# Kernel tuning notes

Hardware: AMD Instinct MI355X
Metric: run time of the kernel (lower is better)

## Reference

```python
import jax, jax.numpy as jnp
import numpy as np

L, B, S, D, H, DH, I, M = 4, 8, 1024, 256, 8, 32, 1024, 4
EPS = 1e-12


def setup_inputs() -> dict:
    key = jax.random.key(0)
    ks = jax.random.split(key, 12)

    def nrm(k, shape, scale=0.02):
        return jax.random.normal(k, shape, jnp.float32) * scale

    x = jax.random.randint(ks[0], (B, S), 0, M + 1)  # POVM outcome tokens + start token

    # sinusoidal positional encoding buffer [S, D]
    pos = np.arange(S, dtype=np.float32)[:, None]
    div = np.exp(np.arange(0, D, 2, dtype=np.float32) * (-np.log(10000.0) / D))
    pe_np = np.zeros((S, D), np.float32)
    pe_np[:, 0::2] = np.sin(pos * div)
    pe_np[:, 1::2] = np.cos(pos * div)

    return {
        "x": x,
        "emb_w": nrm(ks[1], (M + 1, D)),
        "pe": jnp.asarray(pe_np),
        "q_w": nrm(ks[2], (L, D, D)), "q_b": jnp.zeros((L, D)),
        "k_w": nrm(ks[3], (L, D, D)), "k_b": jnp.zeros((L, D)),
        "v_w": nrm(ks[4], (L, D, D)), "v_b": jnp.zeros((L, D)),
        "o_w": nrm(ks[5], (L, D, D)), "o_b": jnp.zeros((L, D)),
        "ln1_g": jnp.ones((L, D)), "ln1_b": jnp.zeros((L, D)),
        "f1_w": nrm(ks[6], (L, I, D)), "f1_b": jnp.zeros((L, I)),
        "f2_w": nrm(ks[7], (L, D, I)), "f2_b": jnp.zeros((L, D)),
        "ln2_g": jnp.ones((L, D)), "ln2_b": jnp.zeros((L, D)),
        "out_w": nrm(ks[8], (M, D)), "out_b": jnp.zeros((M,)),
    }


def _ln(x, g, b):
    m = jnp.mean(x, -1, keepdims=True)
    v = jnp.mean((x - m) ** 2, -1, keepdims=True)
    return g * (x - m) * jax.lax.rsqrt(v + EPS) + b


def reference(x, emb_w, pe, q_w, q_b, k_w, k_b, v_w, v_b, o_w, o_b,
              ln1_g, ln1_b, f1_w, f1_b, f2_w, f2_b, ln2_g, ln2_b,
              out_w, out_b):
    h = emb_w[x] + pe[None, :S, :]                       # [B,S,D]
    mask = jnp.triu(jnp.full((S, S), -1e9, jnp.float32), 1)  # causal look-ahead
    scale = 1.0 / jnp.sqrt(jnp.float32(DH))

    for l in range(L):
        # multi-head self-attention (torch Linear: x @ W.T + b)
        q = (h @ q_w[l].T + q_b[l]).reshape(B, S, H, DH)
        k = (h @ k_w[l].T + k_b[l]).reshape(B, S, H, DH)
        v = (h @ v_w[l].T + v_b[l]).reshape(B, S, H, DH)
        scores = jnp.einsum('bqhd,bkhd->bhqk', q, k) * scale + mask
        probs = jax.nn.softmax(scores, axis=-1)
        ctx = jnp.einsum('bhqk,bkhd->bqhd', probs, v).reshape(B, S, D)
        attn_out = _ln(ctx @ o_w[l].T + o_b[l] + h, ln1_g[l], ln1_b[l])
        # feed-forward sublayer
        ff = jax.nn.gelu(attn_out @ f1_w[l].T + f1_b[l], approximate=False)
        h = _ln(ff @ f2_w[l].T + f2_b[l] + attn_out, ln2_g[l], ln2_b[l])

    logits = h @ out_w.T + out_b                          # [B,S,M]
    return logits
```

## Files before the change

kernel.cpp:

```cpp
#include <hip/hip_runtime.h>
#include <cstdint>
#include <cstddef>

#define SS 1024
#define DD 256

typedef unsigned short u16;
typedef __bf16 bf16x8 __attribute__((ext_vector_type(8)));
typedef float f32x4 __attribute__((ext_vector_type(4)));
typedef unsigned short us4 __attribute__((ext_vector_type(4)));

typedef __attribute__((address_space(3))) void lds_void_t;
typedef __attribute__((address_space(1))) const void gvoid_t;

__device__ __forceinline__ u16 f2bf(float f) {
  unsigned u = __builtin_bit_cast(unsigned, f);
  u += 0x7fffu + ((u >> 16) & 1u);
  return (u16)(u >> 16);
}
__device__ __forceinline__ u16 f2bf_fast(float f) {
  unsigned u = __builtin_bit_cast(unsigned, f) + 0x8000u;
  return (u16)(u >> 16);
}
__device__ __forceinline__ float bf2f(u16 h) {
  return __builtin_bit_cast(float, ((unsigned)h) << 16);
}
__device__ __forceinline__ void gld_lds16(const void* g, void* l) {
  __builtin_amdgcn_global_load_lds((gvoid_t*)g, (lds_void_t*)l, 16, 0, 0);
}
template <int CTRL>
__device__ __forceinline__ float dppf(float x) {
  int i = __builtin_bit_cast(int, x);
  int r = __builtin_amdgcn_update_dpp(i, i, CTRL, 0xf, 0xf, false);
  return __builtin_bit_cast(float, r);
}
__device__ __forceinline__ float row_sum16(float v) {
  v += dppf<0x121>(v);
  v += dppf<0x122>(v);
  v += dppf<0x124>(v);
  v += dppf<0x128>(v);
  return v;
}

struct CvtArgs {
  const float* src[9];
  void* dst[9];
  int n4[9];
  int bf[9];
};

__global__ __launch_bounds__(256) void cvt_kernel(CvtArgs a) {
  int g = blockIdx.y;
  int i = blockIdx.x * 256 + threadIdx.x;
  if (i >= a.n4[g]) return;
  float4 v = ((const float4*)a.src[g])[i];
  if (a.bf[g]) {
    us4 o; o.x = f2bf(v.x); o.y = f2bf(v.y); o.z = f2bf(v.z); o.w = f2bf(v.w);
    ((us4*)a.dst[g])[i] = o;
  } else {
    ((float4*)a.dst[g])[i] = v;
  }
}

__global__ __launch_bounds__(256)
void embed_kernel(const int* __restrict__ x, const float* __restrict__ emb,
                  const float* __restrict__ pe, u16* __restrict__ h) {
  int wave = threadIdx.x >> 6, lane = threadIdx.x & 63;
  int row = blockIdx.x * 4 + wave;
  int s = row & (SS - 1);
  int tok = x[row];
  float4 e = *(const float4*)(emb + (size_t)tok * DD + lane * 4);
  float4 p = *(const float4*)(pe + (size_t)s * DD + lane * 4);
  us4 o; o.x = f2bf(e.x + p.x); o.y = f2bf(e.y + p.y);
  o.z = f2bf(e.z + p.z); o.w = f2bf(e.w + p.w);
  *(us4*)(h + (size_t)row * DD + lane * 4) = o;
}

enum { EPI_BIAS = 0, EPI_GELU = 1 };

#define Q_SCALE (0.17677669529663689f * 1.4426950408889634f)

template <int BM, int BN, int EPI, bool QKV>
__global__ __launch_bounds__(256)
void gemm_kernel(const u16* __restrict__ A, const u16* __restrict__ W,
                 const float* __restrict__ bias, void* __restrict__ outp,
                 u16* __restrict__ vt_out, int M, int N, int K) {
  const int n0 = blockIdx.x * BN;
  const int m0 = blockIdx.y * BM;
  const int tid = threadIdx.x;
  const int lane = tid & 63;
  const int l15 = lane & 15;
  const int quad = lane >> 4;
  const int wave = tid >> 6;
  const int wrow = wave >> 1, wcol = wave & 1;
  constexpr int WN = BN / 2;
  constexpr int NT = WN / 16;

  const u16* Wp = W;
  const float* biasp = bias;
  u16* out16 = (u16*)outp;
  int zid = 0;
  if constexpr (QKV) {
    zid = blockIdx.z;
    Wp += (size_t)zid * 262144;
    biasp += (size_t)zid * 1024;
    out16 += (size_t)zid * 2097152;
  }

  __shared__ __align__(16) u16 lds[(BM + BN) * 64];
  char* ldsA = (char*)lds;
  char* ldsB = (char*)lds + BM * 128;

  const f32x4 fzero = {0.f, 0.f, 0.f, 0.f};
  f32x4 acc[4][NT];
#pragma unroll
  for (int i = 0; i < 4; ++i)
#pragma unroll
    for (int j = 0; j < NT; ++j) acc[i][j] = fzero;

  for (int kb = 0; kb < K; kb += 64) {
    __syncthreads();
#pragma unroll
    for (int r = 0; r < BM * 8 / 256; ++r) {
      int c = r * 256 + tid;
      int row = c >> 3, slot = c & 7;
      int gc = slot ^ (row & 7);
      gld_lds16((const char*)(A + (size_t)(m0 + row) * K + kb) + gc * 16,
                ldsA + c * 16);
    }
#pragma unroll
    for (int r = 0; r < BN * 8 / 256; ++r) {
      int c = r * 256 + tid;
      int row = c >> 3, slot = c & 7;
      int gc = slot ^ (row & 7);
      gld_lds16((const char*)(Wp + (size_t)(n0 + row) * K + kb) + gc * 16,
                ldsB + c * 16);
    }
    __syncthreads();
#pragma unroll
    for (int kk = 0; kk < 2; ++kk) {
      bf16x8 af[4], bfr[NT];
#pragma unroll
      for (int i = 0; i < 4; ++i) {
        int row = wrow * 64 + i * 16 + l15;
        int slot = (kk * 4 + quad) ^ (row & 7);
        af[i] = *(const bf16x8*)(ldsA + row * 128 + slot * 16);
      }
#pragma unroll
      for (int j = 0; j < NT; ++j) {
        int row = wcol * WN + j * 16 + l15;
        int slot = (kk * 4 + quad) ^ (row & 7);
        bfr[j] = *(const bf16x8*)(ldsB + row * 128 + slot * 16);
      }
#pragma unroll
      for (int i = 0; i < 4; ++i)
#pragma unroll
        for (int j = 0; j < NT; ++j)
          acc[i][j] = __builtin_amdgcn_mfma_f32_16x16x32_bf16(af[i], bfr[j],
                                                              acc[i][j], 0, 0, 0);
    }
  }
  if (QKV && zid == 2) {
#pragma unroll
    for (int i = 0; i < 4; ++i) {
      int rbase = m0 + wrow * 64 + i * 16 + quad * 4;
      int bidx = rbase >> 10, s0 = rbase & 1023;
#pragma unroll
      for (int j = 0; j < NT; ++j) {
        int col = n0 + wcol * WN + j * 16 + l15;
        float bj = biasp[col];
        us4 o;
        o.x = f2bf(acc[i][j][0] + bj);
        o.y = f2bf(acc[i][j][1] + bj);
        o.z = f2bf(acc[i][j][2] + bj);
        o.w = f2bf(acc[i][j][3] + bj);
        *(us4*)(vt_out + ((size_t)(bidx * 8 + (col >> 5)) * 32 + (col & 31)) * SS + s0) = o;
      }
    }
    return;
  }
  const float oscale = (QKV && zid == 0) ? Q_SCALE : 1.0f;
#pragma unroll
  for (int i = 0; i < 4; ++i) {
    int rbase = m0 + wrow * 64 + i * 16 + quad * 4;
#pragma unroll
    for (int j = 0; j < NT; ++j) {
      int col = n0 + wcol * WN + j * 16 + l15;
      float bj = biasp[col];
#pragma unroll
      for (int r = 0; r < 4; ++r) {
        size_t idx = (size_t)(rbase + r) * N + col;
        float v = acc[i][j][r] + bj;
        if constexpr (EPI == EPI_GELU) {
          v = 0.5f * v * (1.0f + erff(v * 0.70710678118654752f));
          out16[idx] = f2bf(v);
        } else {
          out16[idx] = f2bf(v * oscale);
        }
      }
    }
  }
}

template <int K, bool LAST>
__global__ __launch_bounds__(256)
void gemmln_kernel(const u16* __restrict__ A, const u16* __restrict__ W,
                   const float* __restrict__ bias, const u16* __restrict__ res,
                   const float* __restrict__ g, const float* __restrict__ bta,
                   u16* __restrict__ out, const float* __restrict__ ow,
                   const float* __restrict__ obias, float* __restrict__ outp) {
  const int m0 = blockIdx.x * 32;
  const int tid = threadIdx.x;
  const int l15 = tid & 15;
  const int quad = (tid & 63) >> 4;
  const int wave = tid >> 6;

  __shared__ __align__(16) u16 lds[(32 + 256) * 64];
  char* ldsA = (char*)lds;
  char* ldsB = (char*)lds + 32 * 128;

  const f32x4 fzero = {0.f, 0.f, 0.f, 0.f};
  f32x4 acc[2][4];
#pragma unroll
  for (int i = 0; i < 2; ++i)
#pragma unroll
    for (int j = 0; j < 4; ++j) acc[i][j] = fzero;

  for (int kb = 0; kb < K; kb += 64) {
    __syncthreads();
    {
      int c = tid;
      int row = c >> 3, slot = c & 7;
      int gc = slot ^ (row & 7);
      gld_lds16((const char*)(A + (size_t)(m0 + row) * K + kb) + gc * 16,
                ldsA + c * 16);
    }
#pragma unroll
    for (int r = 0; r < 8; ++r) {
      int c = r * 256 + tid;
      int row = c >> 3, slot = c & 7;
      int gc = slot ^ (row & 7);
      gld_lds16((const char*)(W + (size_t)row * K + kb) + gc * 16,
                ldsB + c * 16);
    }
    __syncthreads();
#pragma unroll
    for (int kk = 0; kk < 2; ++kk) {
      bf16x8 af[2], bfr[4];
#pragma unroll
      for (int i = 0; i < 2; ++i) {
        int row = i * 16 + l15;
        int slot = (kk * 4 + quad) ^ (row & 7);
        af[i] = *(const bf16x8*)(ldsA + row * 128 + slot * 16);
      }
#pragma unroll
      for (int j = 0; j < 4; ++j) {
        int row = wave * 64 + j * 16 + l15;
        int slot = (kk * 4 + quad) ^ (row & 7);
        bfr[j] = *(const bf16x8*)(ldsB + row * 128 + slot * 16);
      }
#pragma unroll
      for (int i = 0; i < 2; ++i)
#pragma unroll
        for (int j = 0; j < 4; ++j)
          acc[i][j] = __builtin_amdgcn_mfma_f32_16x16x32_bf16(af[i], bfr[j],
                                                              acc[i][j], 0, 0, 0);
    }
  }
  float sm[2][4], sq[2][4];
#pragma unroll
  for (int i = 0; i < 2; ++i)
#pragma unroll
    for (int r = 0; r < 4; ++r) { sm[i][r] = 0.f; sq[i][r] = 0.f; }
#pragma unroll
  for (int j = 0; j < 4; ++j) {
    int col = wave * 64 + j * 16 + l15;
    float bj = bias[col];
#pragma unroll
    for (int i = 0; i < 2; ++i) {
#pragma unroll
      for (int r = 0; r < 4; ++r) {
        int grow = m0 + i * 16 + quad * 4 + r;
        float v = acc[i][j][r] + bj + bf2f(res[(size_t)grow * DD + col]);
        acc[i][j][r] = v;
        sm[i][r] += v;
        sq[i][r] += v * v;
      }
    }
  }
#pragma unroll
  for (int i = 0; i < 2; ++i)
#pragma unroll
    for (int r = 0; r < 4; ++r) {
      sm[i][r] = row_sum16(sm[i][r]);
      sq[i][r] = row_sum16(sq[i][r]);
    }
  __syncthreads();
  float* sred = (float*)lds;
  if (l15 == 0) {
#pragma unroll
    for (int i = 0; i < 2; ++i)
#pragma unroll
      for (int r = 0; r < 4; ++r) {
        int ri = i * 16 + quad * 4 + r;
        sred[wave * 64 + ri] = sm[i][r];
        sred[wave * 64 + 32 + ri] = sq[i][r];
      }
  }
  __syncthreads();
  float mean[2][4], rstd[2][4];
#pragma unroll
  for (int i = 0; i < 2; ++i)
#pragma unroll
    for (int r = 0; r < 4; ++r) {
      int ri = i * 16 + quad * 4 + r;
      float S = sred[ri] + sred[64 + ri] + sred[128 + ri] + sred[192 + ri];
      float S2 = sred[32 + ri] + sred[96 + ri] + sred[160 + ri] + sred[224 + ri];
      float mu = S * (1.f / 256.f);
      mean[i][r] = mu;
      rstd[i][r] = rsqrtf(S2 * (1.f / 256.f) - mu * mu + 1e-12f);
    }
  if constexpr (!LAST) {
#pragma unroll
    for (int j = 0; j < 4; ++j) {
      int col = wave * 64 + j * 16 + l15;
      float gj = g[col], bj = bta[col];
#pragma unroll
      for (int i = 0; i < 2; ++i)
#pragma unroll
        for (int r = 0; r < 4; ++r) {
          int grow = m0 + i * 16 + quad * 4 + r;
          float v = (acc[i][j][r] - mean[i][r]) * rstd[i][r] * gj + bj;
          out[(size_t)grow * DD + col] = f2bf(v);
        }
    }
  } else {
    float lg[2][4][4];
#pragma unroll
    for (int i = 0; i < 2; ++i)
#pragma unroll
      for (int r = 0; r < 4; ++r)
#pragma unroll
        for (int m = 0; m < 4; ++m) lg[i][r][m] = 0.f;
#pragma unroll
    for (int j = 0; j < 4; ++j) {
      int col = wave * 64 + j * 16 + l15;
      float gj = g[col], bj = bta[col];
      float wm[4];
#pragma unroll
      for (int m = 0; m < 4; ++m) wm[m] = ow[m * 256 + col];
#pragma unroll
      for (int i = 0; i < 2; ++i)
#pragma unroll
        for (int r = 0; r < 4; ++r) {
          float v = (acc[i][j][r] - mean[i][r]) * rstd[i][r] * gj + bj;
#pragma unroll
          for (int m = 0; m < 4; ++m) lg[i][r][m] += v * wm[m];
        }
    }
#pragma unroll
    for (int i = 0; i < 2; ++i)
#pragma unroll
      for (int r = 0; r < 4; ++r)
#pragma unroll
        for (int m = 0; m < 4; ++m) lg[i][r][m] = row_sum16(lg[i][r][m]);
    __syncthreads();
    float* sredh = (float*)lds;
    if (l15 == 0) {
#pragma unroll
      for (int i = 0; i < 2; ++i)
#pragma unroll
        for (int r = 0; r < 4; ++r)
#pragma unroll
          for (int m = 0; m < 4; ++m)
            sredh[wave * 128 + (i * 16 + quad * 4 + r) * 4 + m] = lg[i][r][m];
    }
    __syncthreads();
    if (tid < 128) {
      int rr = tid >> 2, m = tid & 3;
      float s = sredh[rr * 4 + m] + sredh[128 + rr * 4 + m] +
                sredh[256 + rr * 4 + m] + sredh[384 + rr * 4 + m] + obias[m];
      outp[(size_t)(m0 + rr) * 4 + m] = s;
    }
  }
}

__global__ __launch_bounds__(256)
void attn_kernel(const u16* __restrict__ Q, const u16* __restrict__ Km,
                 const u16* __restrict__ Vt, u16* __restrict__ ctx) {
  const int tid = threadIdx.x;
  const int l15 = tid & 15;
  const int quad = (tid & 63) >> 4;
  const int wave = tid >> 6;
  const int y = blockIdx.y;
  const int qt = 15 - (((int)blockIdx.x + ((y >> 4) << 2)) & 15);
  const int q0 = qt * 64;
  const int b = y >> 3, h = y & 7;
  const int q0w = q0 + wave * 16;

  __shared__ __align__(16) u16 sK[2][64 * 40];
  __shared__ __align__(16) u16 sV[2][32 * 72];
  __shared__ __align__(16) u16 sP[4][16 * 72];
  u16* sPw = sP[wave];

  bf16x8 qf = *(const bf16x8*)(Q + ((size_t)(b * SS + q0w + l15)) * DD + h * 32 + quad * 8);

  const int krow = tid >> 2, kch = tid & 3;
  const int vd = tid >> 3, vch = tid & 7;
  const u16* Kbase = Km + (size_t)(b * SS) * DD + h * 32;
  const u16* Vbase = Vt + ((size_t)y * 32 + vd) * SS;

  uint4 kreg = *(const uint4*)(Kbase + (size_t)krow * DD + kch * 8);
  uint4 vreg = *(const uint4*)(Vbase + vch * 8);

  f32x4 o0 = {0.f, 0.f, 0.f, 0.f}, o1 = {0.f, 0.f, 0.f, 0.f};
  const f32x4 fzero = {0.f, 0.f, 0.f, 0.f};
  float rs[4] = {0.f, 0.f, 0.f, 0.f};

  const int nt = q0 >> 6;
  for (int it = 0; it <= nt; ++it) {
    const int bsel = it & 1;
    *(uint4*)((char*)sK[bsel] + krow * 80 + kch * 16) = kreg;
    *(uint4*)((char*)sV[bsel] + vd * 144 + vch * 16) = vreg;
    if (it < nt) {
      int kb = (it + 1) * 64;
      kreg = *(const uint4*)(Kbase + (size_t)(kb + krow) * DD + kch * 8);
      vreg = *(const uint4*)(Vbase + kb + vch * 8);
    }
    __syncthreads();

    f32x4 s4[4];
#pragma unroll
    for (int t = 0; t < 4; ++t) {
      bf16x8 kf = *(const bf16x8*)((const char*)sK[bsel] + (t * 16 + l15) * 80 + quad * 16);
      s4[t] = __builtin_amdgcn_mfma_f32_16x16x32_bf16(qf, kf, fzero, 0, 0, 0);
    }
    if (it == nt) {
#pragma unroll
      for (int t = 0; t < 4; ++t) {
        int key = it * 64 + t * 16 + l15;
#pragma unroll
        for (int r = 0; r < 4; ++r) {
          int qr = q0w + quad * 4 + r;
          float p = exp2f(s4[t][r]);
          p = (key > qr) ? 0.f : p;
          s4[t][r] = p;
          rs[r] += p;
        }
      }
    } else {
#pragma unroll
      for (int t = 0; t < 4; ++t)
#pragma unroll
        for (int r = 0; r < 4; ++r) {
          float p = exp2f(s4[t][r]);
          s4[t][r] = p;
          rs[r] += p;
        }
    }
#pragma unroll
    for (int t = 0; t < 4; ++t)
#pragma unroll
      for (int r = 0; r < 4; ++r)
        sPw[(quad * 4 + r) * 72 + t * 16 + l15] = f2bf_fast(s4[t][r]);
#pragma unroll
    for (int kt = 0; kt < 2; ++kt) {
      bf16x8 pf = *(const bf16x8*)((char*)sPw + l15 * 144 + kt * 64 + quad * 16);
      bf16x8 v0 = *(const bf16x8*)((const char*)sV[bsel] + l15 * 144 + kt * 64 + quad * 16);
      bf16x8 v1 = *(const bf16x8*)((const char*)sV[bsel] + (16 + l15) * 144 + kt * 64 + quad * 16);
      o0 = __builtin_amdgcn_mfma_f32_16x16x32_bf16(pf, v0, o0, 0, 0, 0);
      o1 = __builtin_amdgcn_mfma_f32_16x16x32_bf16(pf, v1, o1, 0, 0, 0);
    }
  }
#pragma unroll
  for (int r = 0; r < 4; ++r) {
    float inv = 1.0f / row_sum16(rs[r]);
    int q = q0w + quad * 4 + r;
    size_t base = ((size_t)(b * SS + q)) * DD + h * 32;
    ctx[base + l15] = f2bf(o0[r] * inv);
    ctx[base + 16 + l15] = f2bf(o1[r] * inv);
  }
}

extern "C" void kernel_launch(void* const* d_in, const int* in_sizes, int n_in,
                              void* d_out, int out_size, void* d_ws, size_t ws_size,
                              hipStream_t stream) {
  const int* x = (const int*)d_in[0];
  const float* emb_w = (const float*)d_in[1];
  const float* pe = (const float*)d_in[2];
  const float* q_w = (const float*)d_in[3];
  const float* q_b = (const float*)d_in[4];
  const float* k_w = (const float*)d_in[5];
  const float* k_b = (const float*)d_in[6];
  const float* v_w = (const float*)d_in[7];
  const float* v_b = (const float*)d_in[8];
  const float* o_w = (const float*)d_in[9];
  const float* o_b = (const float*)d_in[10];
  const float* ln1_g = (const float*)d_in[11];
  const float* ln1_b = (const float*)d_in[12];
  const float* f1_w = (const float*)d_in[13];
  const float* f1_b = (const float*)d_in[14];
  const float* f2_w = (const float*)d_in[15];
  const float* f2_b = (const float*)d_in[16];
  const float* ln2_g = (const float*)d_in[17];
  const float* ln2_b = (const float*)d_in[18];
  const float* out_w = (const float*)d_in[19];
  const float* out_b = (const float*)d_in[20];
  float* out = (float*)d_out;

  char* w = (char*)d_ws;
  const size_t MB = 1ull << 20;
  u16* hb    = (u16*)(w + 0 * MB);
  u16* qb    = (u16*)(w + 4 * MB);
  u16* kbuf  = (u16*)(w + 8 * MB);
  u16* vtb   = (u16*)(w + 12 * MB);
  u16* ctxb  = (u16*)(w + 16 * MB);
  u16* attnb = (u16*)(w + 20 * MB);
  u16* ffb   = (u16*)(w + 24 * MB);
  u16* wqkv  = (u16*)(w + 48 * MB);
  u16* wo    = (u16*)(w + 50 * MB);
  u16* wf1   = (u16*)(w + 51 * MB);
  u16* wf2   = (u16*)(w + 53 * MB);
  float* bqkv = (float*)(w + 55 * MB);

  CvtArgs ca;
  ca.src[0] = q_w;  ca.dst[0] = wqkv;            ca.n4[0] = 65536;  ca.bf[0] = 1;
  ca.src[1] = k_w;  ca.dst[1] = wqkv + 262144;   ca.n4[1] = 65536;  ca.bf[1] = 1;
  ca.src[2] = v_w;  ca.dst[2] = wqkv + 524288;   ca.n4[2] = 65536;  ca.bf[2] = 1;
  ca.src[3] = o_w;  ca.dst[3] = wo;              ca.n4[3] = 65536;  ca.bf[3] = 1;
  ca.src[4] = f1_w; ca.dst[4] = wf1;             ca.n4[4] = 262144; ca.bf[4] = 1;
  ca.src[5] = f2_w; ca.dst[5] = wf2;             ca.n4[5] = 262144; ca.bf[5] = 1;
  ca.src[6] = q_b;  ca.dst[6] = bqkv;            ca.n4[6] = 256;    ca.bf[6] = 0;
  ca.src[7] = k_b;  ca.dst[7] = bqkv + 1024;     ca.n4[7] = 256;    ca.bf[7] = 0;
  ca.src[8] = v_b;  ca.dst[8] = bqkv + 2048;     ca.n4[8] = 256;    ca.bf[8] = 0;
  cvt_kernel<<<dim3(1024, 9), 256, 0, stream>>>(ca);

  embed_kernel<<<2048, 256, 0, stream>>>(x, emb_w, pe, hb);

  for (int l = 0; l < 4; ++l) {
    const size_t wofs = (size_t)l * 65536;
    const size_t fofs = (size_t)l * 262144;
    gemm_kernel<128, 64, EPI_BIAS, true><<<dim3(4, 64, 3), 256, 0, stream>>>(
        hb, wqkv + wofs, bqkv + l * 256, qb, vtb, 8192, 256, 256);
    attn_kernel<<<dim3(16, 64), 256, 0, stream>>>(qb, kbuf, vtb, ctxb);
    gemmln_kernel<256, false><<<256, 256, 0, stream>>>(
        ctxb, wo + wofs, o_b + l * 256, hb, ln1_g + l * 256, ln1_b + l * 256,
        attnb, nullptr, nullptr, nullptr);
    gemm_kernel<128, 128, EPI_GELU, false><<<dim3(8, 64), 256, 0, stream>>>(
        attnb, wf1 + fofs, f1_b + l * 1024, ffb, nullptr, 8192, 1024, 256);
    if (l < 3) {
      gemmln_kernel<1024, false><<<256, 256, 0, stream>>>(
          ffb, wf2 + fofs, f2_b + l * 256, attnb, ln2_g + l * 256,
          ln2_b + l * 256, hb, nullptr, nullptr, nullptr);
    } else {
      gemmln_kernel<1024, true><<<256, 256, 0, stream>>>(
          ffb, wf2 + fofs, f2_b + l * 256, attnb, ln2_g + l * 256,
          ln2_b + l * 256, hb, out_w, out_b, out);
    }
  }
}
```

Measured before the change: 392.4 us.

## Double attention query tile per block and widen gemmln K-step to 128

The attention kernel now handles 128 query rows per block as two 64-row halves that share each staged K/V tile, which halves the grid and the K/V global loads. A mirrored query-tile order is kept to balance the causal work. Separately, the fused GEMM+LayerNorm kernel stages 128-wide K slices instead of 64, doubling LDS use per block but halving the number of barriers per K loop. The risks are lower occupancy from more LDS and registers, fewer blocks for the attention pass, and more load imbalance because the causal work per block is now coarser.

```diff
diff --git a/kernel.cpp b/kernel.cpp
--- a/kernel.cpp
+++ b/kernel.cpp
@@ -215,9 +215,9 @@
   const int quad = (tid & 63) >> 4;
   const int wave = tid >> 6;
 
-  __shared__ __align__(16) u16 lds[(32 + 256) * 64];
+  __shared__ __align__(16) u16 lds[(32 + 256) * 128];
   char* ldsA = (char*)lds;
-  char* ldsB = (char*)lds + 32 * 128;
+  char* ldsB = (char*)lds + 32 * 256;
 
   const f32x4 fzero = {0.f, 0.f, 0.f, 0.f};
   f32x4 acc[2][4];
@@ -226,38 +226,39 @@
 #pragma unroll
     for (int j = 0; j < 4; ++j) acc[i][j] = fzero;
 
-  for (int kb = 0; kb < K; kb += 64) {
+  for (int kb = 0; kb < K; kb += 128) {
     __syncthreads();
-    {
-      int c = tid;
-      int row = c >> 3, slot = c & 7;
+#pragma unroll
+    for (int r = 0; r < 2; ++r) {
+      int c = r * 256 + tid;
+      int row = c >> 4, slot = c & 15;
       int gc = slot ^ (row & 7);
       gld_lds16((const char*)(A + (size_t)(m0 + row) * K + kb) + gc * 16,
                 ldsA + c * 16);
     }
 #pragma unroll
-    for (int r = 0; r < 8; ++r) {
+    for (int r = 0; r < 16; ++r) {
       int c = r * 256 + tid;
-      int row = c >> 3, slot = c & 7;
+      int row = c >> 4, slot = c & 15;
       int gc = slot ^ (row & 7);
       gld_lds16((const char*)(W + (size_t)row * K + kb) + gc * 16,
                 ldsB + c * 16);
     }
     __syncthreads();
 #pragma unroll
-    for (int kk = 0; kk < 2; ++kk) {
+    for (int kk = 0; kk < 4; ++kk) {
       bf16x8 af[2], bfr[4];
 #pragma unroll
       for (int i = 0; i < 2; ++i) {
         int row = i * 16 + l15;
         int slot = (kk * 4 + quad) ^ (row & 7);
-        af[i] = *(const bf16x8*)(ldsA + row * 128 + slot * 16);
+        af[i] = *(const bf16x8*)(ldsA + row * 256 + slot * 16);
       }
 #pragma unroll
       for (int j = 0; j < 4; ++j) {
         int row = wave * 64 + j * 16 + l15;
         int slot = (kk * 4 + quad) ^ (row & 7);
-        bfr[j] = *(const bf16x8*)(ldsB + row * 128 + slot * 16);
+        bfr[j] = *(const bf16x8*)(ldsB + row * 256 + slot * 16);
       }
 #pragma unroll
       for (int i = 0; i < 2; ++i)
@@ -393,17 +394,22 @@
   const int quad = (tid & 63) >> 4;
   const int wave = tid >> 6;
   const int y = blockIdx.y;
-  const int qt = 15 - (((int)blockIdx.x + ((y >> 4) << 2)) & 15);
-  const int q0 = qt * 64;
+  const int xb = blockIdx.x;
+  const int qsel = ((y >> 5) & 1) ? (7 - xb) : xb;
+  const int q0 = qsel * 128;
   const int b = y >> 3, h = y & 7;
-  const int q0w = q0 + wave * 16;
 
   __shared__ __align__(16) u16 sK[2][64 * 40];
   __shared__ __align__(16) u16 sV[2][32 * 72];
-  __shared__ __align__(16) u16 sP[4][16 * 72];
-  u16* sPw = sP[wave];
-
-  bf16x8 qf = *(const bf16x8*)(Q + ((size_t)(b * SS + q0w + l15)) * DD + h * 32 + quad * 8);
+  __shared__ __align__(16) u16 sP0[4][16 * 72];
+  __shared__ __align__(16) u16 sP1[4][16 * 72];
+  u16* sPw0 = sP0[wave];
+  u16* sPw1 = sP1[wave];
+
+  const int qr0 = q0 + wave * 16;
+  const int qr1 = q0 + 64 + wave * 16;
+  bf16x8 qf0 = *(const bf16x8*)(Q + ((size_t)(b * SS + qr0 + l15)) * DD + h * 32 + quad * 8);
+  bf16x8 qf1 = *(const bf16x8*)(Q + ((size_t)(b * SS + qr1 + l15)) * DD + h * 32 + quad * 8);
 
   const int krow = tid >> 2, kch = tid & 3;
   const int vd = tid >> 3, vch = tid & 7;
@@ -413,11 +419,12 @@
   uint4 kreg = *(const uint4*)(Kbase + (size_t)krow * DD + kch * 8);
   uint4 vreg = *(const uint4*)(Vbase + vch * 8);
 
-  f32x4 o0 = {0.f, 0.f, 0.f, 0.f}, o1 = {0.f, 0.f, 0.f, 0.f};
+  f32x4 o00 = {0.f, 0.f, 0.f, 0.f}, o01 = {0.f, 0.f, 0.f, 0.f};
+  f32x4 o10 = {0.f, 0.f, 0.f, 0.f}, o11 = {0.f, 0.f, 0.f, 0.f};
   const f32x4 fzero = {0.f, 0.f, 0.f, 0.f};
-  float rs[4] = {0.f, 0.f, 0.f, 0.f};
-
-  const int nt = q0 >> 6;
+  float rs0[4] = {0.f, 0.f, 0.f, 0.f}, rs1[4] = {0.f, 0.f, 0.f, 0.f};
+
+  const int nt = (q0 >> 6) + 1;
   for (int it = 0; it <= nt; ++it) {
     const int bsel = it & 1;
     *(uint4*)((char*)sK[bsel] + krow * 80 + kch * 16) = kreg;
@@ -429,56 +436,107 @@
     }
     __syncthreads();
 
-    f32x4 s4[4];
-#pragma unroll
-    for (int t = 0; t < 4; ++t) {
-      bf16x8 kf = *(const bf16x8*)((const char*)sK[bsel] + (t * 16 + l15) * 80 + quad * 16);
-      s4[t] = __builtin_amdgcn_mfma_f32_16x16x32_bf16(qf, kf, fzero, 0, 0, 0);
-    }
-    if (it == nt) {
+    if (it < nt) {
+      f32x4 s4[4];
 #pragma unroll
       for (int t = 0; t < 4; ++t) {
-        int key = it * 64 + t * 16 + l15;
-#pragma unroll
-        for (int r = 0; r < 4; ++r) {
-          int qr = q0w + quad * 4 + r;
-          float p = exp2f(s4[t][r]);
-          p = (key > qr) ? 0.f : p;
-          s4[t][r] = p;
-          rs[r] += p;
+        bf16x8 kf = *(const bf16x8*)((const char*)sK[bsel] + (t * 16 + l15) * 80 + quad * 16);
+        s4[t] = __builtin_amdgcn_mfma_f32_16x16x32_bf16(qf0, kf, fzero, 0, 0, 0);
+      }
+      if (it == nt - 1) {
+#pragma unroll
+        for (int t = 0; t < 4; ++t) {
+          int key = it * 64 + t * 16 + l15;
+#pragma unroll
+          for (int r = 0; r < 4; ++r) {
+            int qr = qr0 + quad * 4 + r;
+            float p = exp2f(s4[t][r]);
+            p = (key > qr) ? 0.f : p;
+            s4[t][r] = p;
+            rs0[r] += p;
+          }
         }
-      }
-    } else {
+      } else {
+#pragma unroll
+        for (int t = 0; t < 4; ++t)
+#pragma unroll
+          for (int r = 0; r < 4; ++r) {
+            float p = exp2f(s4[t][r]);
+            s4[t][r] = p;
+            rs0[r] += p;
+          }
+      }
 #pragma unroll
       for (int t = 0; t < 4; ++t)
 #pragma unroll
-        for (int r = 0; r < 4; ++r) {
-          float p = exp2f(s4[t][r]);
-          s4[t][r] = p;
-          rs[r] += p;
+        for (int r = 0; r < 4; ++r)
+          sPw0[(quad * 4 + r) * 72 + t * 16 + l15] = f2bf_fast(s4[t][r]);
+#pragma unroll
+      for (int kt = 0; kt < 2; ++kt) {
+        bf16x8 pf = *(const bf16x8*)((char*)sPw0 + l15 * 144 + kt * 64 + quad * 16);
+        bf16x8 v0 = *(const bf16x8*)((const char*)sV[bsel] + l15 * 144 + kt * 64 + quad * 16);
+        bf16x8 v1 = *(const bf16x8*)((const char*)sV[bsel] + (16 + l15) * 144 + kt * 64 + quad * 16);
+        o00 = __builtin_amdgcn_mfma_f32_16x16x32_bf16(pf, v0, o00, 0, 0, 0);
+        o01 = __builtin_amdgcn_mfma_f32_16x16x32_bf16(pf, v1, o01, 0, 0, 0);
+      }
+    }
+    {
+      f32x4 s4[4];
+#pragma unroll
+      for (int t = 0; t < 4; ++t) {
+        bf16x8 kf = *(const bf16x8*)((const char*)sK[bsel] + (t * 16 + l15) * 80 + quad * 16);
+        s4[t] = __builtin_amdgcn_mfma_f32_16x16x32_bf16(qf1, kf, fzero, 0, 0, 0);
+      }
+      if (it == nt) {
+#pragma unroll
+        for (int t = 0; t < 4; ++t) {
+          int key = it * 64 + t * 16 + l15;
+#pragma unroll
+          for (int r = 0; r < 4; ++r) {
+            int qr = qr1 + quad * 4 + r;
+            float p = exp2f(s4[t][r]);
+            p = (key > qr) ? 0.f : p;
+            s4[t][r] = p;
+            rs1[r] += p;
+          }
         }
-    }
-#pragma unroll
-    for (int t = 0; t < 4; ++t)
-#pragma unroll
-      for (int r = 0; r < 4; ++r)
-        sPw[(quad * 4 + r) * 72 + t * 16 + l15] = f2bf_fast(s4[t][r]);
-#pragma unroll
-    for (int kt = 0; kt < 2; ++kt) {
-      bf16x8 pf = *(const bf16x8*)((char*)sPw + l15 * 144 + kt * 64 + quad * 16);
-      bf16x8 v0 = *(const bf16x8*)((const char*)sV[bsel] + l15 * 144 + kt * 64 + quad * 16);
-      bf16x8 v1 = *(const bf16x8*)((const char*)sV[bsel] + (16 + l15) * 144 + kt * 64 + quad * 16);
-      o0 = __builtin_amdgcn_mfma_f32_16x16x32_bf16(pf, v0, o0, 0, 0, 0);
-      o1 = __builtin_amdgcn_mfma_f32_16x16x32_bf16(pf, v1, o1, 0, 0, 0);
+      } else {
+#pragma unroll
+        for (int t = 0; t < 4; ++t)
+#pragma unroll
+          for (int r = 0; r < 4; ++r) {
+            float p = exp2f(s4[t][r]);
+            s4[t][r] = p;
+            rs1[r] += p;
+          }
+      }
+#pragma unroll
+      for (int t = 0; t < 4; ++t)
+#pragma unroll
+        for (int r = 0; r < 4; ++r)
+          sPw1[(quad * 4 + r) * 72 + t * 16 + l15] = f2bf_fast(s4[t][r]);
+#pragma unroll
+      for (int kt = 0; kt < 2; ++kt) {
+        bf16x8 pf = *(const bf16x8*)((char*)sPw1 + l15 * 144 + kt * 64 + quad * 16);
+        bf16x8 v0 = *(const bf16x8*)((const char*)sV[bsel] + l15 * 144 + kt * 64 + quad * 16);
+        bf16x8 v1 = *(const bf16x8*)((const char*)sV[bsel] + (16 + l15) * 144 + kt * 64 + quad * 16);
+        o10 = __builtin_amdgcn_mfma_f32_16x16x32_bf16(pf, v0, o10, 0, 0, 0);
+        o11 = __builtin_amdgcn_mfma_f32_16x16x32_bf16(pf, v1, o11, 0, 0, 0);
+      }
     }
   }
 #pragma unroll
   for (int r = 0; r < 4; ++r) {
-    float inv = 1.0f / row_sum16(rs[r]);
-    int q = q0w + quad * 4 + r;
-    size_t base = ((size_t)(b * SS + q)) * DD + h * 32;
-    ctx[base + l15] = f2bf(o0[r] * inv);
-    ctx[base + 16 + l15] = f2bf(o1[r] * inv);
+    float inv0 = 1.0f / row_sum16(rs0[r]);
+    float inv1 = 1.0f / row_sum16(rs1[r]);
+    int qa = qr0 + quad * 4 + r;
+    int qb2 = qr1 + quad * 4 + r;
+    size_t base0 = ((size_t)(b * SS + qa)) * DD + h * 32;
+    size_t base1 = ((size_t)(b * SS + qb2)) * DD + h * 32;
+    ctx[base0 + l15] = f2bf(o00[r] * inv0);
+    ctx[base0 + 16 + l15] = f2bf(o01[r] * inv0);
+    ctx[base1 + l15] = f2bf(o10[r] * inv1);
+    ctx[base1 + 16 + l15] = f2bf(o11[r] * inv1);
   }
 }
 
@@ -542,7 +600,7 @@
     const size_t fofs = (size_t)l * 262144;
     gemm_kernel<128, 64, EPI_BIAS, true><<<dim3(4, 64, 3), 256, 0, stream>>>(
         hb, wqkv + wofs, bqkv + l * 256, qb, vtb, 8192, 256, 256);
-    attn_kernel<<<dim3(16, 64), 256, 0, stream>>>(qb, kbuf, vtb, ctxb);
+    attn_kernel<<<dim3(8, 64), 256, 0, stream>>>(qb, kbuf, vtb, ctxb);
     gemmln_kernel<256, false><<<256, 256, 0, stream>>>(
         ctxb, wo + wofs, o_b + l * 256, hb, ln1_g + l * 256, ln1_b + l * 256,
         attnb, nullptr, nullptr, nullptr);
```

Measured after the change: 402.6 us. +2.6%, slower.
